# Performance work log

Hardware: AMD Instinct MI355X
Metric: run time of the kernel (lower is better)

## Reference

```python
import jax, jax.numpy as jnp
import numpy as np

N, H, W, C = 4, 64, 64, 256
G, K = 8, 3
GC = C // G
P = K * K
PAD = 1
BN_EPS = 1e-3  # ultralytics Conv uses BatchNorm2d(eps=0.001)


def setup_inputs() -> dict:
    key = jax.random.key(0)
    ks = jax.random.split(key, 8)
    return {
        "x": jax.random.normal(ks[0], (N, H, W, C), jnp.float32),
        # depthwise conv weight (OIHW with I=1, feature_group_count=C)
        "dw_w": jax.random.normal(ks[1], (C, 1, K, K), jnp.float32) * 0.1,
        "bn_gamma": jnp.ones((C,), jnp.float32),
        "bn_beta": jnp.zeros((C,), jnp.float32),
        "bn_mean": jnp.zeros((C,), jnp.float32),
        "bn_var": jnp.ones((C,), jnp.float32),
        # offset/mask heads are zero-init in torch; use small random weights so
        # sampling locations are nontrivial but stay near the kernel grid
        "W_off": jax.random.normal(ks[2], (C, G * P * 2), jnp.float32) * 0.01,
        "b_off": jnp.zeros((G * P * 2,), jnp.float32),
        "W_mask": jax.random.normal(ks[3], (C, G * P), jnp.float32) * 0.01,
        "b_mask": jnp.zeros((G * P,), jnp.float32),
        "W_in": jax.random.normal(ks[4], (C, C), jnp.float32) / np.sqrt(C).astype(np.float32),
        "b_in": jnp.zeros((C,), jnp.float32),
        "W_out": jax.random.normal(ks[5], (C, C), jnp.float32) / np.sqrt(C).astype(np.float32),
        "b_out": jnp.zeros((C,), jnp.float32),
    }


def _grid_sample(img, grid):
    # img: (B, gc, Hi, Wi); grid: (B, L, P, 2) in [-1,1], (x,y) order.
    # Matches torch grid_sample(mode='bilinear', padding_mode='zeros', align_corners=False).
    B, gc, Hi, Wi = img.shape
    x = (grid[..., 0] + 1.0) * (Wi * 0.5) - 0.5
    y = (grid[..., 1] + 1.0) * (Hi * 0.5) - 0.5
    x0 = jnp.floor(x).astype(jnp.int32)
    y0 = jnp.floor(y).astype(jnp.int32)
    tx = x - x0
    ty = y - y0
    flat = img.reshape(B, gc, Hi * Wi)
    L, Pp = grid.shape[1], grid.shape[2]

    def tap(xi, yi, w):
        valid = (xi >= 0) & (xi < Wi) & (yi >= 0) & (yi < Hi)
        idx = jnp.clip(yi, 0, Hi - 1) * Wi + jnp.clip(xi, 0, Wi - 1)
        v = jnp.take_along_axis(flat, idx.reshape(B, 1, L * Pp), axis=2)
        v = v.reshape(B, gc, L, Pp)
        return v * (w * valid)[:, None]

    return (tap(x0, y0, (1 - tx) * (1 - ty))
            + tap(x0 + 1, y0, tx * (1 - ty))
            + tap(x0, y0 + 1, (1 - tx) * ty)
            + tap(x0 + 1, y0 + 1, tx * ty))


def _dcnv3_core(xp, offset, mask):
    # xp: (N,H,W,C) projected input; offset: (N,H,W,G*P*2); mask: (N,H,W,G*P)
    xpad = jnp.pad(xp, ((0, 0), (PAD, PAD), (PAD, PAD), (0, 0)))
    Hi, Wi = H + 2 * PAD, W + 2 * PAD
    # reference points on the padded grid, normalized to [0,1]
    start = (K - 1) // 2 + 0.5  # dilation=1, stride=1
    ref_y = (start + jnp.arange(H, dtype=jnp.float32)) / Hi
    ref_x = (start + jnp.arange(W, dtype=jnp.float32)) / Wi
    ref = jnp.stack(jnp.broadcast_arrays(ref_x[None, :], ref_y[:, None]), -1)  # (H,W,2) (x,y)
    # kernel dilation grid; torch meshgrid('ij') over (kw,kh) -> point p = iw*K + ih
    xv = jnp.arange(K, dtype=jnp.float32) - ((K - 1) // 2)
    gx, gy = jnp.meshgrid(xv / Wi, xv / Hi, indexing='ij')
    kgrid = jnp.stack([gx, gy], -1).reshape(P, 2)  # identical per group
    off = offset.reshape(N, H, W, G, P, 2) / jnp.array([Wi, Hi], jnp.float32)
    loc = ref[None, :, :, None, None, :] + kgrid[None, None, None, None] + off  # (N,H,W,G,P,2)
    sg = 2.0 * loc - 1.0
    # regroup channels-last input to (N*G, GC, Hi, Wi); channel c = g*GC + d
    img = xpad.reshape(N, Hi * Wi, G, GC).transpose(0, 2, 3, 1).reshape(N * G, GC, Hi, Wi)
    sgrid = sg.reshape(N, H * W, G, P, 2).transpose(0, 2, 1, 3, 4).reshape(N * G, H * W, P, 2)
    samp = _grid_sample(img, sgrid)  # (N*G, GC, L, P)
    m = mask.reshape(N, H * W, G, P).transpose(0, 2, 1, 3).reshape(N * G, 1, H * W, P)
    out = (samp * m).sum(-1)  # (N*G, GC, L)
    return out.reshape(N, C, H * W).transpose(0, 2, 1).reshape(N, H, W, C)


def reference(x, dw_w, bn_gamma, bn_beta, bn_mean, bn_var, W_off, b_off,
              W_mask, b_mask, W_in, b_in, W_out, b_out):
    x_proj = x @ W_in + b_in
    # depthwise 3x3 conv + BN (eval) + SiLU (ultralytics Conv)
    xc = x.transpose(0, 3, 1, 2)
    y = jax.lax.conv_general_dilated(
        xc, dw_w, (1, 1), ((PAD, PAD), (PAD, PAD)),
        feature_group_count=C, dimension_numbers=('NCHW', 'OIHW', 'NCHW'))
    scale = bn_gamma / jnp.sqrt(bn_var + BN_EPS)
    y = (y - bn_mean[None, :, None, None]) * scale[None, :, None, None] + bn_beta[None, :, None, None]
    y = y * jax.nn.sigmoid(y)
    x1 = y.transpose(0, 2, 3, 1)  # (N,H,W,C)
    offset = x1 @ W_off + b_off
    mlog = (x1 @ W_mask + b_mask).reshape(N, H, W, G, P)
    mask = jax.nn.softmax(mlog, axis=-1).reshape(N, H, W, G * P)
    out = _dcnv3_core(x_proj, offset, mask)
    return out @ W_out + b_out
```

## Files before the change

### kernel.cpp

```cpp
#include <hip/hip_runtime.h>
#include <math.h>

#define NPIX 16384
#define CC 256
#define OFFW 144
#define MSKW 72

typedef unsigned short ushortT;
typedef __attribute__((ext_vector_type(4))) float f32x4;
typedef __attribute__((ext_vector_type(8))) __bf16 bf16x8;
typedef __attribute__((ext_vector_type(8))) unsigned short u16x8;

__device__ __forceinline__ float bf2f(ushortT u) {
    union { unsigned u; float f; } x; x.u = ((unsigned)u) << 16; return x.f;
}
__device__ __forceinline__ ushortT f2bf(float f) {
    union { float f; unsigned u; } x; x.f = f;
    unsigned u = x.u;
    return (ushortT)((u + 0x7FFFu + ((u >> 16) & 1u)) >> 16);
}

typedef __attribute__((address_space(3))) char lds_char;
typedef __attribute__((address_space(1))) char glb_char;
__device__ __forceinline__ void gload_lds16(const void* g, void* l) {
    __builtin_amdgcn_global_load_lds((const glb_char*)g, (lds_char*)l, 16, 0, 0);
}

__global__ __launch_bounds__(256) void k_wt(
    const float* __restrict__ W_in, const float* __restrict__ W_out,
    const float* __restrict__ W_off, const float* __restrict__ W_mask,
    const float* __restrict__ b_in, const float* __restrict__ b_out,
    const float* __restrict__ b_off, const float* __restrict__ b_mask,
    ushortT* __restrict__ Wt, float* __restrict__ biasb)
{
    const int idx = blockIdx.x * 256 + threadIdx.x;
    const int slot = idx >> 16;
    const int rem = idx & 65535;
    const int n = rem >> 8, k = rem & 255;
    float v;
    if (slot == 0)      v = W_in[k * 256 + n];
    else if (slot == 1) v = W_out[k * 256 + n];
    else {
        if (n < OFFW)             v = W_off[k * OFFW + n];
        else if (n < OFFW + MSKW) v = W_mask[k * MSKW + (n - OFFW)];
        else                      v = 0.f;
    }
    Wt[idx] = f2bf(v);
    if (n == 0) {
        float b;
        if (slot == 0)      b = b_in[k];
        else if (slot == 1) b = b_out[k];
        else                b = (k < OFFW) ? b_off[k] : (k < OFFW + MSKW ? b_mask[k - OFFW] : 0.f);
        biasb[slot * 256 + k] = b;
    }
}

__global__ __launch_bounds__(512, 4) void k_fused_in(
    const float* __restrict__ x, const float* __restrict__ dw_w,
    const float* __restrict__ bn_gamma, const float* __restrict__ bn_beta,
    const float* __restrict__ bn_mean, const float* __restrict__ bn_var,
    const ushortT* __restrict__ Wt, const float* __restrict__ biasb,
    float* __restrict__ xpf, float* __restrict__ om)
{
    __shared__ __align__(16) ushortT xA[32 * 256];
    __shared__ __align__(16) ushortT x1s[32 * 256];
    const int tid = threadIdx.x;
    const int b0 = blockIdx.x;
    const int lb = (b0 & 7) * 64 + (b0 >> 3);
    const int base = lb * 32;
    const int n = base >> 12, h = (base >> 6) & 63, bw0 = base & 63;

    {
        const int c = tid & 255, half = tid >> 8;
        float wreg[9];
        #pragma unroll
        for (int k = 0; k < 9; ++k) wreg[k] = dw_w[c * 9 + k];
        const float scale = bn_gamma[c] * rsqrtf(bn_var[c] + 1e-3f);
        const float mean = bn_mean[c], beta = bn_beta[c];
        const bool hv0 = h >= 1, hv2 = h <= 62;
        const float* r0 = x + ((size_t)(n * 64 + h - 1) * 64) * 256 + c;
        const float* r1 = x + ((size_t)(n * 64 + h) * 64) * 256 + c;
        const float* r2 = x + ((size_t)(n * 64 + h + 1) * 64) * 256 + c;
        const int w0 = bw0 + half * 16;
        float a0, a1, a2, e0, e1, e2;
        if (w0 - 1 >= 0) {
            a0 = hv0 ? r0[(w0 - 1) * 256] : 0.f;
            a1 = r1[(w0 - 1) * 256];
            a2 = hv2 ? r2[(w0 - 1) * 256] : 0.f;
        } else { a0 = a1 = a2 = 0.f; }
        e0 = hv0 ? r0[w0 * 256] : 0.f;
        e1 = r1[w0 * 256];
        e2 = hv2 ? r2[w0 * 256] : 0.f;
        #pragma unroll
        for (int i = 0; i < 16; ++i) {
            const int w = w0 + i;
            float d0, d1, d2;
            if (w + 1 < 64) {
                d0 = hv0 ? r0[(w + 1) * 256] : 0.f;
                d1 = r1[(w + 1) * 256];
                d2 = hv2 ? r2[(w + 1) * 256] : 0.f;
            } else { d0 = d1 = d2 = 0.f; }
            const float accv = a0 * wreg[0] + e0 * wreg[1] + d0 * wreg[2]
                             + a1 * wreg[3] + e1 * wreg[4] + d1 * wreg[5]
                             + a2 * wreg[6] + e2 * wreg[7] + d2 * wreg[8];
            const float yv = (accv - mean) * scale + beta;
            const float s = yv / (1.f + __expf(-yv));
            const int row = half * 16 + i;
            const int sb = (row * 512 + c * 2) ^ ((row & 7) << 4);
            *(ushortT*)((char*)x1s + sb) = f2bf(s);
            *(ushortT*)((char*)xA + sb) = f2bf(e1);
            a0 = e0; a1 = e1; a2 = e2;
            e0 = d0; e1 = d1; e2 = d2;
        }
    }
    __syncthreads();

    const int lane = tid & 63, wave = tid >> 6;
    const int gemm = wave >> 2, wc = wave & 3;
    const ushortT* As = gemm ? x1s : xA;
    const ushortT* Bt = Wt + (gemm ? 2 * 65536 : 0);
    const float* bias = biasb + (gemm ? 512 : 0);
    float* Cout = gemm ? om : xpf;

    f32x4 acc[2][4];
    #pragma unroll
    for (int m = 0; m < 2; ++m)
        #pragma unroll
        for (int nn = 0; nn < 4; ++nn) acc[m][nn] = (f32x4){0.f, 0.f, 0.f, 0.f};

    #pragma unroll
    for (int k0 = 0; k0 < 256; k0 += 32) {
        bf16x8 af[2], bb[4];
        #pragma unroll
        for (int m = 0; m < 2; ++m) {
            const int row = m * 16 + (lane & 15);
            af[m] = *(const bf16x8*)((const char*)As + row * 512 +
                     (((k0 + (lane >> 4) * 8) * 2) ^ ((row & 7) << 4)));
        }
        #pragma unroll
        for (int nn = 0; nn < 4; ++nn) {
            const int ncol = wc * 64 + nn * 16 + (lane & 15);
            bb[nn] = *(const bf16x8*)(Bt + (size_t)ncol * 256 + k0 + (lane >> 4) * 8);
        }
        #pragma unroll
        for (int m = 0; m < 2; ++m)
            #pragma unroll
            for (int nn = 0; nn < 4; ++nn)
                acc[m][nn] = __builtin_amdgcn_mfma_f32_16x16x32_bf16(af[m], bb[nn], acc[m][nn], 0, 0, 0);
    }

    const int rbase = (lane >> 4) * 4, col16 = lane & 15;
    #pragma unroll
    for (int m = 0; m < 2; ++m) {
        #pragma unroll
        for (int nn = 0; nn < 4; ++nn) {
            const int col = wc * 64 + nn * 16 + col16;
            const float bj = bias[col];
            #pragma unroll
            for (int r = 0; r < 4; ++r) {
                const int row = m * 16 + rbase + r;
                Cout[(size_t)(base + row) * 256 + col] = acc[m][nn][r] + bj;
            }
        }
    }
}

__global__ __launch_bounds__(256) void k_core(
    const float* __restrict__ om, const float* __restrict__ xpf,
    ushortT* __restrict__ coreb)
{
    __shared__ __align__(16) float wtab[8][72][8];
    const int tid = threadIdx.x;
    const int b0 = blockIdx.x;
    const int lb = (b0 & 7) * 256 + (b0 >> 3);
    const int base = lb * 8;
    const int n = base >> 12, h = (base >> 6) & 63, w0 = base & 63;

    if (tid < 64) {
        const int px = tid >> 3, g = tid & 7;
        const float* omp = om + (size_t)(base + px) * 256;
        float lg[9], mx = -1e30f;
        #pragma unroll
        for (int p = 0; p < 9; ++p) { lg[p] = omp[OFFW + g * 9 + p]; mx = fmaxf(mx, lg[p]); }
        float e[9], sum = 0.f;
        #pragma unroll
        for (int p = 0; p < 9; ++p) { e[p] = __expf(lg[p] - mx); sum += e[p]; }
        const float inv = 1.f / sum;
        #pragma unroll
        for (int p = 0; p < 9; ++p) {
            const float m = e[p] * inv;
            const float ox = omp[(g * 9 + p) * 2], oy = omp[(g * 9 + p) * 2 + 1];
            const float pxc = (float)(w0 + px + p / 3) + ox;
            const float pyc = (float)(h + p % 3) + oy;
            const float xf = floorf(pxc), yf = floorf(pyc);
            const float tx = pxc - xf, ty = pyc - yf;
            const int x0 = (int)xf - 1, y0 = (int)yf - 1;
            const int x1 = x0 + 1, y1 = y0 + 1;
            const float wx0 = ((unsigned)x0 < 64u) ? (1.f - tx) : 0.f;
            const float wx1 = ((unsigned)x1 < 64u) ? tx : 0.f;
            const float wy0 = ((unsigned)y0 < 64u) ? (1.f - ty) : 0.f;
            const float wy1 = ((unsigned)y1 < 64u) ? ty : 0.f;
            const int cx0 = min(max(x0, 0), 63), cx1 = min(max(x1, 0), 63);
            const int cy0 = min(max(y0, 0), 63), cy1 = min(max(y1, 0), 63);
            float* dst = wtab[px][g * 9 + p];
            float4 idx4, wt4;
            idx4.x = __int_as_float((cy0 * 64 + cx0) * 256);
            idx4.y = __int_as_float((cy0 * 64 + cx1) * 256);
            idx4.z = __int_as_float((cy1 * 64 + cx0) * 256);
            idx4.w = __int_as_float((cy1 * 64 + cx1) * 256);
            wt4.x = m * wx0 * wy0; wt4.y = m * wx1 * wy0;
            wt4.z = m * wx0 * wy1; wt4.w = m * wx1 * wy1;
            *(float4*)dst = idx4;
            *(float4*)(dst + 4) = wt4;
        }
    }
    __syncthreads();

    const int px = tid >> 5, g = (tid >> 2) & 7, o = tid & 3;
    const float* xn = xpf + (size_t)n * (4096 * 256) + g * 32 + o * 8;
    float acc[8];
    #pragma unroll
    for (int j = 0; j < 8; ++j) acc[j] = 0.f;
    #pragma unroll
    for (int p = 0; p < 9; ++p) {
        const float* wt = wtab[px][g * 9 + p];
        const int4 o4 = *(const int4*)(wt);
        const float4 w4 = *(const float4*)(wt + 4);
        const f32x4 a0 = *(const f32x4*)(xn + o4.x);
        const f32x4 a1 = *(const f32x4*)(xn + o4.x + 4);
        const f32x4 b0 = *(const f32x4*)(xn + o4.y);
        const f32x4 b1 = *(const f32x4*)(xn + o4.y + 4);
        const f32x4 c0 = *(const f32x4*)(xn + o4.z);
        const f32x4 c1 = *(const f32x4*)(xn + o4.z + 4);
        const f32x4 d0 = *(const f32x4*)(xn + o4.w);
        const f32x4 d1 = *(const f32x4*)(xn + o4.w + 4);
        #pragma unroll
        for (int j = 0; j < 4; ++j) {
            acc[j]     += w4.x * a0[j] + w4.y * b0[j] + w4.z * c0[j] + w4.w * d0[j];
            acc[4 + j] += w4.x * a1[j] + w4.y * b1[j] + w4.z * c1[j] + w4.w * d1[j];
        }
    }
    u16x8 cv;
    #pragma unroll
    for (int j = 0; j < 8; ++j) cv[j] = f2bf(acc[j]);
    *(u16x8*)(coreb + (size_t)(base + px) * 256 + g * 32 + o * 8) = cv;
}

__global__ __launch_bounds__(256) void k_gemm_out(
    const ushortT* __restrict__ A, const ushortT* __restrict__ Bt,
    const float* __restrict__ bias, float* __restrict__ out)
{
    __shared__ __align__(16) ushortT As[64 * 256];
    const int tid = threadIdx.x;
    const int m0 = blockIdx.x * 64;
    const int lane = tid & 63, wave = tid >> 6;

    #pragma unroll
    for (int it = 0; it < 16; ++it) {
        const int i = it * 256 + tid;
        const int row = i >> 5, ch = i & 31;
        const int sch = ch ^ (row & 7);
        gload_lds16(A + (size_t)(m0 + row) * 256 + sch * 8, (char*)As + i * 16);
    }
    asm volatile("s_waitcnt vmcnt(0)");
    __syncthreads();

    f32x4 acc[4][4];
    #pragma unroll
    for (int m = 0; m < 4; ++m)
        #pragma unroll
        for (int nn = 0; nn < 4; ++nn) acc[m][nn] = (f32x4){0.f, 0.f, 0.f, 0.f};

    #pragma unroll
    for (int k0 = 0; k0 < 256; k0 += 32) {
        bf16x8 af[4], bb[4];
        #pragma unroll
        for (int m = 0; m < 4; ++m) {
            const int row = m * 16 + (lane & 15);
            af[m] = *(const bf16x8*)((const char*)As + row * 512 +
                     (((k0 + (lane >> 4) * 8) * 2) ^ ((row & 7) << 4)));
        }
        #pragma unroll
        for (int nn = 0; nn < 4; ++nn) {
            const int ncol = wave * 64 + nn * 16 + (lane & 15);
            bb[nn] = *(const bf16x8*)(Bt + (size_t)ncol * 256 + k0 + (lane >> 4) * 8);
        }
        #pragma unroll
        for (int m = 0; m < 4; ++m)
            #pragma unroll
            for (int nn = 0; nn < 4; ++nn)
                acc[m][nn] = __builtin_amdgcn_mfma_f32_16x16x32_bf16(af[m], bb[nn], acc[m][nn], 0, 0, 0);
    }

    const int rbase = (lane >> 4) * 4, col16 = lane & 15;
    #pragma unroll
    for (int m = 0; m < 4; ++m) {
        #pragma unroll
        for (int nn = 0; nn < 4; ++nn) {
            const int col = wave * 64 + nn * 16 + col16;
            const float bj = bias[col];
            #pragma unroll
            for (int r = 0; r < 4; ++r) {
                const int row = m0 + m * 16 + rbase + r;
                out[(size_t)row * 256 + col] = acc[m][nn][r] + bj;
            }
        }
    }
}

extern "C" void kernel_launch(void* const* d_in, const int* in_sizes, int n_in,
                              void* d_out, int out_size, void* d_ws, size_t ws_size,
                              hipStream_t stream) {
    const float* x        = (const float*)d_in[0];
    const float* dw_w     = (const float*)d_in[1];
    const float* bn_gamma = (const float*)d_in[2];
    const float* bn_beta  = (const float*)d_in[3];
    const float* bn_mean  = (const float*)d_in[4];
    const float* bn_var   = (const float*)d_in[5];
    const float* W_off    = (const float*)d_in[6];
    const float* b_off    = (const float*)d_in[7];
    const float* W_mask   = (const float*)d_in[8];
    const float* b_mask   = (const float*)d_in[9];
    const float* W_in     = (const float*)d_in[10];
    const float* b_in     = (const float*)d_in[11];
    const float* W_out    = (const float*)d_in[12];
    const float* b_out    = (const float*)d_in[13];
    float* out = (float*)d_out;

    char* w = (char*)d_ws;
    ushortT* Wt    = (ushortT*)w;
    float* biasb   = (float*)(w + 393216);
    float* xpf     = (float*)(w + 396288);
    float* om      = (float*)(w + 396288 + 16777216);
    ushortT* coreb = (ushortT*)(w + 396288 + 2 * 16777216);

    hipLaunchKernelGGL(k_wt, dim3(768), dim3(256), 0, stream,
                       W_in, W_out, W_off, W_mask, b_in, b_out, b_off, b_mask, Wt, biasb);
    hipLaunchKernelGGL(k_fused_in, dim3(512), dim3(512), 0, stream,
                       x, dw_w, bn_gamma, bn_beta, bn_mean, bn_var, Wt, biasb, xpf, om);
    hipLaunchKernelGGL(k_core, dim3(2048), dim3(256), 0, stream,
                       om, xpf, coreb);
    hipLaunchKernelGGL(k_gemm_out, dim3(NPIX / 64), dim3(256), 0, stream,
                       coreb, Wt + 65536, biasb + 256, out);
}
```

Baseline: 71.07 us.

## Store projected input as bf16 for the sampling gather and halve output GEMM tile

The input projection result is now written as bf16 instead of fp32. The deformable sampling kernel gathers 16-byte bf16 vectors per corner instead of two fp32 vectors and unpacks them with shifts, which halves gather traffic and workspace. Separately, the output GEMM uses 32-row tiles instead of 64, doubling the block count so more CUs are busy. The cost is extra rounding of the sampled values, plus less reuse of the B operand per block in the output GEMM.

```diff
diff --git a/kernel.cpp b/kernel.cpp
--- a/kernel.cpp
+++ b/kernel.cpp
@@ -10,6 +10,7 @@
 typedef __attribute__((ext_vector_type(4))) float f32x4;
 typedef __attribute__((ext_vector_type(8))) __bf16 bf16x8;
 typedef __attribute__((ext_vector_type(8))) unsigned short u16x8;
+typedef __attribute__((ext_vector_type(4))) unsigned int u32x4;
 
 __device__ __forceinline__ float bf2f(ushortT u) {
     union { unsigned u; float f; } x; x.u = ((unsigned)u) << 16; return x.f;
@@ -19,6 +20,8 @@
     unsigned u = x.u;
     return (ushortT)((u + 0x7FFFu + ((u >> 16) & 1u)) >> 16);
 }
+__device__ __forceinline__ float bflo(unsigned u) { return __uint_as_float(u << 16); }
+__device__ __forceinline__ float bfhi(unsigned u) { return __uint_as_float(u & 0xFFFF0000u); }
 
 typedef __attribute__((address_space(3))) char lds_char;
 typedef __attribute__((address_space(1))) char glb_char;
@@ -60,7 +63,7 @@
     const float* __restrict__ bn_gamma, const float* __restrict__ bn_beta,
     const float* __restrict__ bn_mean, const float* __restrict__ bn_var,
     const ushortT* __restrict__ Wt, const float* __restrict__ biasb,
-    float* __restrict__ xpf, float* __restrict__ om)
+    ushortT* __restrict__ xpb, float* __restrict__ om)
 {
     __shared__ __align__(16) ushortT xA[32 * 256];
     __shared__ __align__(16) ushortT x1s[32 * 256];
@@ -120,7 +123,6 @@
     const ushortT* As = gemm ? x1s : xA;
     const ushortT* Bt = Wt + (gemm ? 2 * 65536 : 0);
     const float* bias = biasb + (gemm ? 512 : 0);
-    float* Cout = gemm ? om : xpf;
 
     f32x4 acc[2][4];
     #pragma unroll
@@ -159,14 +161,16 @@
             #pragma unroll
             for (int r = 0; r < 4; ++r) {
                 const int row = m * 16 + rbase + r;
-                Cout[(size_t)(base + row) * 256 + col] = acc[m][nn][r] + bj;
+                const float v = acc[m][nn][r] + bj;
+                if (gemm == 0) xpb[(size_t)(base + row) * 256 + col] = f2bf(v);
+                else           om[(size_t)(base + row) * 256 + col] = v;
             }
         }
     }
 }
 
 __global__ __launch_bounds__(256) void k_core(
-    const float* __restrict__ om, const float* __restrict__ xpf,
+    const float* __restrict__ om, const ushortT* __restrict__ xpb,
     ushortT* __restrict__ coreb)
 {
     __shared__ __align__(16) float wtab[8][72][8];
@@ -217,7 +221,7 @@
     __syncthreads();
 
     const int px = tid >> 5, g = (tid >> 2) & 7, o = tid & 3;
-    const float* xn = xpf + (size_t)n * (4096 * 256) + g * 32 + o * 8;
+    const ushortT* xn = xpb + (size_t)n * (4096 * 256) + g * 32 + o * 8;
     float acc[8];
     #pragma unroll
     for (int j = 0; j < 8; ++j) acc[j] = 0.f;
@@ -226,18 +230,16 @@
         const float* wt = wtab[px][g * 9 + p];
         const int4 o4 = *(const int4*)(wt);
         const float4 w4 = *(const float4*)(wt + 4);
-        const f32x4 a0 = *(const f32x4*)(xn + o4.x);
-        const f32x4 a1 = *(const f32x4*)(xn + o4.x + 4);
-        const f32x4 b0 = *(const f32x4*)(xn + o4.y);
-        const f32x4 b1 = *(const f32x4*)(xn + o4.y + 4);
-        const f32x4 c0 = *(const f32x4*)(xn + o4.z);
-        const f32x4 c1 = *(const f32x4*)(xn + o4.z + 4);
-        const f32x4 d0 = *(const f32x4*)(xn + o4.w);
-        const f32x4 d1 = *(const f32x4*)(xn + o4.w + 4);
-        #pragma unroll
-        for (int j = 0; j < 4; ++j) {
-            acc[j]     += w4.x * a0[j] + w4.y * b0[j] + w4.z * c0[j] + w4.w * d0[j];
-            acc[4 + j] += w4.x * a1[j] + w4.y * b1[j] + w4.z * c1[j] + w4.w * d1[j];
+        const u32x4 A = *(const u32x4*)(xn + o4.x);
+        const u32x4 B = *(const u32x4*)(xn + o4.y);
+        const u32x4 C = *(const u32x4*)(xn + o4.z);
+        const u32x4 D = *(const u32x4*)(xn + o4.w);
+        #pragma unroll
+        for (int i = 0; i < 4; ++i) {
+            acc[2 * i]     += w4.x * bflo(A[i]) + w4.y * bflo(B[i])
+                            + w4.z * bflo(C[i]) + w4.w * bflo(D[i]);
+            acc[2 * i + 1] += w4.x * bfhi(A[i]) + w4.y * bfhi(B[i])
+                            + w4.z * bfhi(C[i]) + w4.w * bfhi(D[i]);
         }
     }
     u16x8 cv;
@@ -250,13 +252,13 @@
     const ushortT* __restrict__ A, const ushortT* __restrict__ Bt,
     const float* __restrict__ bias, float* __restrict__ out)
 {
-    __shared__ __align__(16) ushortT As[64 * 256];
+    __shared__ __align__(16) ushortT As[32 * 256];
     const int tid = threadIdx.x;
-    const int m0 = blockIdx.x * 64;
+    const int m0 = blockIdx.x * 32;
     const int lane = tid & 63, wave = tid >> 6;
 
     #pragma unroll
-    for (int it = 0; it < 16; ++it) {
+    for (int it = 0; it < 4; ++it) {
         const int i = it * 256 + tid;
         const int row = i >> 5, ch = i & 31;
         const int sch = ch ^ (row & 7);
@@ -265,17 +267,17 @@
     asm volatile("s_waitcnt vmcnt(0)");
     __syncthreads();
 
-    f32x4 acc[4][4];
-    #pragma unroll
-    for (int m = 0; m < 4; ++m)
+    f32x4 acc[2][4];
+    #pragma unroll
+    for (int m = 0; m < 2; ++m)
         #pragma unroll
         for (int nn = 0; nn < 4; ++nn) acc[m][nn] = (f32x4){0.f, 0.f, 0.f, 0.f};
 
     #pragma unroll
     for (int k0 = 0; k0 < 256; k0 += 32) {
-        bf16x8 af[4], bb[4];
-        #pragma unroll
-        for (int m = 0; m < 4; ++m) {
+        bf16x8 af[2], bb[4];
+        #pragma unroll
+        for (int m = 0; m < 2; ++m) {
             const int row = m * 16 + (lane & 15);
             af[m] = *(const bf16x8*)((const char*)As + row * 512 +
                      (((k0 + (lane >> 4) * 8) * 2) ^ ((row & 7) << 4)));
@@ -286,7 +288,7 @@
             bb[nn] = *(const bf16x8*)(Bt + (size_t)ncol * 256 + k0 + (lane >> 4) * 8);
         }
         #pragma unroll
-        for (int m = 0; m < 4; ++m)
+        for (int m = 0; m < 2; ++m)
             #pragma unroll
             for (int nn = 0; nn < 4; ++nn)
                 acc[m][nn] = __builtin_amdgcn_mfma_f32_16x16x32_bf16(af[m], bb[nn], acc[m][nn], 0, 0, 0);
@@ -294,7 +296,7 @@
 
     const int rbase = (lane >> 4) * 4, col16 = lane & 15;
     #pragma unroll
-    for (int m = 0; m < 4; ++m) {
+    for (int m = 0; m < 2; ++m) {
         #pragma unroll
         for (int nn = 0; nn < 4; ++nn) {
             const int col = wave * 64 + nn * 16 + col16;
@@ -330,16 +332,16 @@
     char* w = (char*)d_ws;
     ushortT* Wt    = (ushortT*)w;
     float* biasb   = (float*)(w + 393216);
-    float* xpf     = (float*)(w + 396288);
-    float* om      = (float*)(w + 396288 + 16777216);
-    ushortT* coreb = (ushortT*)(w + 396288 + 2 * 16777216);
+    ushortT* xpb   = (ushortT*)(w + 396288);
+    float* om      = (float*)(w + 396288 + 8388608);
+    ushortT* coreb = (ushortT*)(w + 396288 + 8388608 + 16777216);
 
     hipLaunchKernelGGL(k_wt, dim3(768), dim3(256), 0, stream,
                        W_in, W_out, W_off, W_mask, b_in, b_out, b_off, b_mask, Wt, biasb);
     hipLaunchKernelGGL(k_fused_in, dim3(512), dim3(512), 0, stream,
-                       x, dw_w, bn_gamma, bn_beta, bn_mean, bn_var, Wt, biasb, xpf, om);
+                       x, dw_w, bn_gamma, bn_beta, bn_mean, bn_var, Wt, biasb, xpb, om);
     hipLaunchKernelGGL(k_core, dim3(2048), dim3(256), 0, stream,
-                       om, xpf, coreb);
-    hipLaunchKernelGGL(k_gemm_out, dim3(NPIX / 64), dim3(256), 0, stream,
+                       om, xpb, coreb);
+    hipLaunchKernelGGL(k_gemm_out, dim3(NPIX / 32), dim3(256), 0, stream,
                        coreb, Wt + 65536, biasb + 256, out);
 }
```

Result: faster. 69.10 us (-2.8%).
